# Performance work log

Measured on AMD Instinct MI355X. Metric: run time of the kernel, lower is better.

## Reference

```python
import jax, jax.numpy as jnp
import numpy as np

W = 5      # window size
H = 4      # num heads (num_channels)
EPS = 1e-6

def rmsnorm(x, w):
    return x * w * jax.lax.rsqrt(jnp.mean(x * x, axis=-1, keepdims=True) + EPS)

def dwconv3d(x, k):
    # x: [B,D0,D1,D2,C], k: [3,3,3,1,C] depthwise 3x3x3 conv, SAME padding
    return jax.lax.conv_general_dilated(
        x, k, (1, 1, 1), 'SAME',
        dimension_numbers=('NDHWC', 'DHWIO', 'NDHWC'),
        feature_group_count=x.shape[-1])

def _part(t):
    # [B,D0,D1,D2,C] -> [B*nw, W^3, C] non-overlapping 3D windows
    B, D0, D1, D2, C = t.shape
    t = t.reshape(B, D0 // W, W, D1 // W, W, D2 // W, W, C)
    t = t.transpose(0, 1, 3, 5, 2, 4, 6, 7)
    return t.reshape(-1, W ** 3, C)

def _unpart(t, B, D0, D1, D2):
    C = t.shape[-1]
    t = t.reshape(B, D0 // W, D1 // W, D2 // W, W, W, W, C)
    t = t.transpose(0, 1, 4, 2, 5, 3, 6, 7)
    return t.reshape(B, D0, D1, D2, C)

def _pool01(t):
    # mean-pool poolable_dims=(0,1) by factor W -> coarse grid
    B, D0, D1, D2, C = t.shape
    return t.reshape(B, D0 // W, W, D1 // W, W, D2, C).mean(axis=(2, 4))

def _mha(q, k, v):
    # q,k,v: [N, L, C] -> [N, L, C] multi-head attention
    N, L, C = q.shape
    dh = C // H
    q = q.reshape(N, L, H, dh)
    k = k.reshape(N, L, H, dh)
    v = v.reshape(N, L, H, dh)
    s = jnp.einsum('nqhd,nkhd->nhqk', q, k) * (1.0 / np.sqrt(dh))
    p = jax.nn.softmax(s, axis=-1)
    return jnp.einsum('nhqk,nkhd->nqhd', p, v).reshape(N, L, C)

def _hier_attn(x, qkv_w, qkv_b, proj_w, proj_b, dw_pre, dw_post, lr_down, lr_up):
    B, D0, D1, D2, C = x.shape
    # conv_position='both': pre depthwise-conv positional term
    xin = x + dwconv3d(x, dw_pre)
    qkv = xin @ qkv_w + qkv_b                     # [B,D0,D1,D2,3C]
    q, k, v = jnp.split(qkv, 3, axis=-1)
    # fine scale: windowed local attention in W^3 blocks
    fine = _unpart(_mha(_part(q), _part(k), _part(v)), B, D0, D1, D2)
    # coarse scale: pool dims (0,1) by W, global attention over coarse tokens
    qc, kc, vc = _pool01(q), _pool01(k), _pool01(v)
    Nc = qc.shape[1] * qc.shape[2] * qc.shape[3]
    oc = _mha(qc.reshape(B, Nc, C), kc.reshape(B, Nc, C), vc.reshape(B, Nc, C))
    oc = oc.reshape(B, D0 // W, D1 // W, D2, C)
    oc = jnp.repeat(jnp.repeat(oc, W, axis=1), W, axis=2)   # upsample to full grid
    # lowrank hierarchical merge of coarse branch into fine branch
    merged = fine + (oc @ lr_down) @ lr_up
    out = merged @ proj_w + proj_b
    out = out + xin                               # attn_residual
    out = out + dwconv3d(out, dw_post)            # post conv position
    return out

def setup_inputs() -> dict:
    key = jax.random.key(0)
    ks = jax.random.split(key, 8)
    B, D0, D1, D2, C = 4, 40, 40, 20, 256
    rank = C // 4
    s = 0.02
    return {
        'x': jax.random.normal(ks[0], (B, D0, D1, D2, C), jnp.float32),
        'norm1_w': jnp.ones((C,), jnp.float32),
        'attn_norm_w': jnp.ones((C,), jnp.float32),
        'qkv_w': jax.random.normal(ks[1], (C, 3 * C), jnp.float32) * s,
        'qkv_b': jnp.zeros((3 * C,), jnp.float32),
        'proj_w': jax.random.normal(ks[2], (C, C), jnp.float32) * s,
        'proj_b': jnp.zeros((C,), jnp.float32),
        'dw_pre': jax.random.normal(ks[3], (3, 3, 3, 1, C), jnp.float32) * s,
        'dw_post': jax.random.normal(ks[4], (3, 3, 3, 1, C), jnp.float32) * s,
        'lr_down': jax.random.normal(ks[5], (C, rank), jnp.float32) * s,
        'lr_up': jax.random.normal(ks[6], (rank, C), jnp.float32) * s,
    }

def reference(x, norm1_w, attn_norm_w, qkv_w, qkv_b, proj_w, proj_b,
              dw_pre, dw_post, lr_down, lr_up) -> jnp.ndarray:
    # x = x + attn_norm(hier_attn(norm1(x)))   (dropout inactive in eval)
    a = _hier_attn(rmsnorm(x, norm1_w), qkv_w, qkv_b, proj_w, proj_b,
                   dw_pre, dw_post, lr_down, lr_up)
    return x + rmsnorm(a, attn_norm_w)
```

## Files before the change

kernel.cpp:

```cpp
#include <hip/hip_runtime.h>

#define D0c 40
#define D1c 40
#define D2c 20
#define NVOX 128000

typedef __attribute__((ext_vector_type(4))) float f4;
typedef __attribute__((ext_vector_type(8))) __bf16 bf8;
typedef __attribute__((ext_vector_type(8))) unsigned short u8s;

static __device__ __forceinline__ unsigned short f2bf(float f) {
  union { float f; unsigned int u; } v; v.f = f;
  unsigned int r = v.u + 0x7fffu + ((v.u >> 16) & 1u);
  return (unsigned short)(r >> 16);
}
static __device__ __forceinline__ float bf2f(unsigned short h) {
  union { unsigned int u; float f; } v; v.u = ((unsigned int)h) << 16;
  return v.f;
}

#define MFMA16(a, b, c) __builtin_amdgcn_mfma_f32_16x16x32_bf16((a), (b), (c), 0, 0, 0)

static __device__ __forceinline__ void gload16(const void* g, void* l) {
  __builtin_amdgcn_global_load_lds((const __attribute__((address_space(1))) unsigned int*)g,
                                   (__attribute__((address_space(3))) unsigned int*)l, 16, 0, 0);
}

#define CONV_LOAD(NB, R)                                                      \
  do {                                                                        \
    _Pragma("unroll") for (int c = 0; c < 9; c++)                             \
        NB[c] = *(const ushort4*)(base[c] + (size_t)(R) * 256);               \
  } while (0)

#define CONV_CONSUME(NB)                                                      \
  do {                                                                        \
    f4 cf[9];                                                                 \
    _Pragma("unroll") for (int c = 0; c < 9; c++) {                           \
      cf[c].x = bf2f(NB[c].x); cf[c].y = bf2f(NB[c].y);                       \
      cf[c].z = bf2f(NB[c].z); cf[c].w = bf2f(NB[c].w);                       \
    }                                                                         \
    _Pragma("unroll") for (int c = 0; c < 9; c++) {                           \
      const f4 w0 = *(const f4*)&wl[(c * 3 + 0) * 256 + c0];                  \
      const f4 w1 = *(const f4*)&wl[(c * 3 + 1) * 256 + c0];                  \
      const f4 w2 = *(const f4*)&wl[(c * 3 + 2) * 256 + c0];                  \
      a0 += w2 * cf[c]; a1 += w1 * cf[c]; a2 += w0 * cf[c];                   \
    }                                                                         \
    a1 += cf[4];                                                              \
  } while (0)

#define CONV_SHIFT()                                                          \
  do { a0 = a1; a1 = a2; a2 = (f4){0.f, 0.f, 0.f, 0.f}; } while (0)

__global__ __launch_bounds__(256) void k_prepw(const float* __restrict__ qkv_w,
                                               const float* __restrict__ proj_w,
                                               unsigned short* __restrict__ wq,
                                               unsigned short* __restrict__ wp,
                                               unsigned short* __restrict__ zpad) {
  if (blockIdx.x == 1024) {
    u8s z = {0, 0, 0, 0, 0, 0, 0, 0};
    for (int i = threadIdx.x; i < 768; i += 256) *(u8s*)(zpad + i * 8) = z;
    return;
  }
  int id = blockIdx.x * 256 + threadIdx.x;
  if (id < 768 * 256) {
    int kk = id & 31, row = (id >> 5) & 127, kc = (id >> 12) & 7, nt = id >> 15;
    int s = kk >> 3, kj = kk & 7;
    int g = s ^ ((row >> 1) & 3);
    int k = kc * 32 + g * 8 + kj;
    int n = nt * 128 + row;
    wq[id] = f2bf(qkv_w[k * 768 + n]);
  } else {
    int j = id - 768 * 256;
    int kk = j & 31, row = (j >> 5) & 127, kc = (j >> 12) & 7, nt = j >> 15;
    int s = kk >> 3, kj = kk & 7;
    int g = s ^ ((row >> 1) & 3);
    int k = kc * 32 + g * 8 + kj;
    int n = nt * 128 + row;
    wp[j] = f2bf(proj_w[k * 256 + n]);
  }
}

__global__ __launch_bounds__(256) void k_rms1(const float* __restrict__ x,
                                              const float* __restrict__ w,
                                              unsigned short* __restrict__ xn) {
  int wv = threadIdx.x >> 6, ln = threadIdx.x & 63;
  int n = blockIdx.x * 4 + wv;
  f4 v = ((const f4*)(x + (size_t)n * 256))[ln];
  float ss = v.x * v.x + v.y * v.y + v.z * v.z + v.w * v.w;
#pragma unroll
  for (int m = 32; m >= 1; m >>= 1) ss += __shfl_xor(ss, m);
  float rs = rsqrtf(ss * (1.f / 256.f) + 1e-6f);
  f4 wv4 = ((const f4*)w)[ln];
  ushort4 o;
  o.x = f2bf(v.x * wv4.x * rs); o.y = f2bf(v.y * wv4.y * rs);
  o.z = f2bf(v.z * wv4.z * rs); o.w = f2bf(v.w * wv4.w * rs);
  ((ushort4*)(xn + (size_t)n * 256))[ln] = o;
}

__global__ __launch_bounds__(256) void k_convpre(const unsigned short* __restrict__ xn,
                                                 const float* __restrict__ dw,
                                                 const unsigned short* __restrict__ zpad,
                                                 unsigned short* __restrict__ xin) {
  __shared__ float wl[6912];
  for (int i = threadIdx.x; i < 6912; i += 256) wl[i] = dw[i];
  __syncthreads();
  int wv = threadIdx.x >> 6, ln = threadIdx.x & 63;
  int col = blockIdx.x * 4 + wv;
  int z1 = col % D1c; int t = col / D1c; int z0 = t % D0c; int b = t / D0c;
  int c0 = ln * 4;

  const unsigned short* base[9];
#pragma unroll
  for (int c = 0; c < 9; c++) {
    int dy = c / 3 - 1, dx = c % 3 - 1;
    int y0 = z0 + dy, y1 = z1 + dx;
    bool valid = ((unsigned)y0 < (unsigned)D0c) && ((unsigned)y1 < (unsigned)D1c);
    base[c] = valid ? (xn + ((size_t)((b * D0c + y0) * D1c + y1) * D2c) * 256 + c0)
                    : (zpad + c0);
  }
  f4 a0 = {0.f,0.f,0.f,0.f}, a1 = {0.f,0.f,0.f,0.f}, a2 = {0.f,0.f,0.f,0.f};
  ushort4 n0[9], n1[9];
  CONV_LOAD(n0, 0);
  CONV_LOAD(n1, 1);
  unsigned short* op = xin + ((size_t)col * D2c) * 256 + c0;

  CONV_CONSUME(n0);
  CONV_SHIFT();
  CONV_LOAD(n0, 2);
  CONV_CONSUME(n1);
  {
    ushort4 o;
    o.x = f2bf(a0.x); o.y = f2bf(a0.y); o.z = f2bf(a0.z); o.w = f2bf(a0.w);
    *(ushort4*)op = o; op += 256;
  }
  CONV_SHIFT();
  CONV_LOAD(n1, 3);

  for (int z = 2; z < 20; z += 2) {
    CONV_CONSUME(n0);
    {
      ushort4 o;
      o.x = f2bf(a0.x); o.y = f2bf(a0.y); o.z = f2bf(a0.z); o.w = f2bf(a0.w);
      *(ushort4*)op = o; op += 256;
    }
    CONV_SHIFT();
    int r2 = (z + 2 > 19) ? 19 : (z + 2);
    CONV_LOAD(n0, r2);

    CONV_CONSUME(n1);
    {
      ushort4 o;
      o.x = f2bf(a0.x); o.y = f2bf(a0.y); o.z = f2bf(a0.z); o.w = f2bf(a0.w);
      *(ushort4*)op = o; op += 256;
    }
    CONV_SHIFT();
    int r3 = (z + 3 > 19) ? 19 : (z + 3);
    CONV_LOAD(n1, r3);
  }
  {
    ushort4 o;
    o.x = f2bf(a0.x); o.y = f2bf(a0.y); o.z = f2bf(a0.z); o.w = f2bf(a0.w);
    *(ushort4*)op = o;
  }
}

__global__ __launch_bounds__(256) void k_gemm_qkv(const unsigned short* __restrict__ a_bf,
                                                  const unsigned short* __restrict__ wq2,
                                                  const float* __restrict__ bias,
                                                  unsigned short* __restrict__ out) {
  __shared__ unsigned short As[16384];
  __shared__ unsigned short Bs[8192];
  int m0 = blockIdx.x * 64;
  int tid = threadIdx.x;
  int w = tid >> 6, l = tid & 63;
  int wr = w >> 1, wc = w & 1;
  int lrow = l & 15, lg = l >> 4;

  {
    const char* Ab = (const char*)(a_bf + (size_t)m0 * 256);
    int row = tid >> 2, s = tid & 3;
    int g = s ^ ((row >> 1) & 3);
    const char* src0 = Ab + row * 512 + g * 16;
    char* dst0 = ((char*)As) + w * 1024 + l * 16;
#pragma unroll
    for (int kc = 0; kc < 8; kc++)
      gload16(src0 + kc * 64, dst0 + kc * 4096);
  }
  {
    const char* gB = (const char*)wq2;
    char* lB = (char*)Bs;
    gload16(gB + tid * 16, lB + w * 1024 + l * 16);
    gload16(gB + 4096 + tid * 16, lB + 4096 + w * 1024 + l * 16);
  }

  int buf = 0;
  f4 acc[2][4];
  for (int nt = 0; nt < 6; nt++) {
    float bvv[4];
#pragma unroll
    for (int j = 0; j < 4; j++) bvv[j] = bias[nt * 128 + wc * 64 + j * 16 + lrow];
#pragma unroll
    for (int i = 0; i < 2; i++)
#pragma unroll
      for (int j = 0; j < 4; j++) acc[i][j] = {0.f, 0.f, 0.f, 0.f};

    for (int kc = 0; kc < 8; kc++) {
      int t = nt * 8 + kc;
      if (t + 1 < 48) {
        const char* gB = (const char*)wq2 + (size_t)(t + 1) * 8192;
        char* lB = ((char*)Bs) + (buf ^ 1) * 8192;
        gload16(gB + tid * 16, lB + w * 1024 + l * 16);
        gload16(gB + 4096 + tid * 16, lB + 4096 + w * 1024 + l * 16);
        asm volatile("s_waitcnt vmcnt(2)\n\ts_barrier" ::: "memory");
      } else {
        asm volatile("s_waitcnt vmcnt(0)\n\ts_barrier" ::: "memory");
      }
      bf8 af[2], bf_[4];
#pragma unroll
      for (int i = 0; i < 2; i++) {
        int row = wr * 32 + i * 16 + lrow;
        af[i] = *(const bf8*)&As[kc * 2048 + row * 32 + ((lg ^ ((row >> 1) & 3)) * 8)];
      }
#pragma unroll
      for (int j = 0; j < 4; j++) {
        int rowb = wc * 64 + j * 16 + lrow;
        bf_[j] = *(const bf8*)&Bs[buf * 4096 + rowb * 32 + ((lg ^ ((rowb >> 1) & 3)) * 8)];
      }
#pragma unroll
      for (int i = 0; i < 2; i++)
#pragma unroll
        for (int j = 0; j < 4; j++) acc[i][j] = MFMA16(af[i], bf_[j], acc[i][j]);
      asm volatile("s_barrier" ::: "memory");
      buf ^= 1;
    }

    unsigned short* Cs = &Bs[(buf ^ 1) * 4096];
    int crow = tid >> 3, cseg = tid & 7;
#pragma unroll
    for (int h = 0; h < 2; h++) {
      if (wr == h) {
#pragma unroll
        for (int i = 0; i < 2; i++)
#pragma unroll
          for (int j = 0; j < 4; j++)
#pragma unroll
            for (int r = 0; r < 4; r++)
              Cs[(i * 16 + lg * 4 + r) * 128 + wc * 64 + j * 16 + lrow] =
                  f2bf(acc[i][j][r] + bvv[j]);
      }
      asm volatile("s_waitcnt lgkmcnt(0)\n\ts_barrier" ::: "memory");
      {
        u8s v0 = *(const u8s*)&Cs[crow * 128 + cseg * 16];
        u8s v1 = *(const u8s*)&Cs[crow * 128 + cseg * 16 + 8];
        unsigned short* orow = out + (size_t)(m0 + h * 32 + crow) * 768 + nt * 128 + cseg * 16;
        *(u8s*)orow = v0;
        *(u8s*)(orow + 8) = v1;
      }
      asm volatile("s_waitcnt lgkmcnt(0)\n\ts_barrier" ::: "memory");
    }
  }
}

__global__ __launch_bounds__(256) void k_fineattn(const unsigned short* __restrict__ qkv,
                                                  unsigned short* __restrict__ fine) {
  __shared__ unsigned short sm[27136];
  unsigned short* Qs = sm;
  unsigned short* Ks = sm + 9216;
  unsigned short* Vt = sm + 18432;
  unsigned short* Ps = sm;
  int h = blockIdx.x & 3, wid = blockIdx.x >> 2;
  int w2 = wid & 3, w1 = (wid >> 2) & 7, w0 = (wid >> 5) & 7, b = wid >> 8;
  int tid = threadIdx.x;
  int tok = tid >> 1, half = tid & 1;
  if (tok < 125) {
    int i0 = tok / 25, rr = tok % 25, i1 = rr / 5, i2 = rr % 5;
    int n = ((b * D0c + w0 * 5 + i0) * D1c + w1 * 5 + i1) * D2c + w2 * 5 + i2;
    const u8s* qp = (const u8s*)(qkv + (size_t)n * 768 + h * 64 + half * 32);
    const u8s* kp = (const u8s*)(qkv + (size_t)n * 768 + 256 + h * 64 + half * 32);
    const unsigned short* vp = qkv + (size_t)n * 768 + 512 + h * 64 + half * 32;
#pragma unroll
    for (int e = 0; e < 4; e++) {
      *(u8s*)&Qs[tok * 72 + half * 32 + e * 8] = qp[e];
      *(u8s*)&Ks[tok * 72 + half * 32 + e * 8] = kp[e];
    }
#pragma unroll
    for (int d = 0; d < 32; d++) Vt[(half * 32 + d) * 136 + tok] = vp[d];
  } else {
    u8s z = {0, 0, 0, 0, 0, 0, 0, 0};
#pragma unroll
    for (int e = 0; e < 4; e++) {
      *(u8s*)&Qs[tok * 72 + half * 32 + e * 8] = z;
      *(u8s*)&Ks[tok * 72 + half * 32 + e * 8] = z;
    }
#pragma unroll
    for (int d = 0; d < 32; d++) Vt[(half * 32 + d) * 136 + tok] = 0;
  }
  __syncthreads();
  int wv = tid >> 6, ln = tid & 63, lrow = ln & 15, lg = ln >> 4;
  f4 s[2][8];
#pragma unroll
  for (int mi = 0; mi < 2; mi++)
#pragma unroll
    for (int ni = 0; ni < 8; ni++) s[mi][ni] = {0.f, 0.f, 0.f, 0.f};
  bf8 aq[2][2];
#pragma unroll
  for (int ks = 0; ks < 2; ks++)
#pragma unroll
    for (int mi = 0; mi < 2; mi++)
      aq[mi][ks] = *(const bf8*)&Qs[(wv * 32 + mi * 16 + lrow) * 72 + ks * 32 + lg * 8];
#pragma unroll
  for (int ni = 0; ni < 8; ni++) {
#pragma unroll
    for (int ks = 0; ks < 2; ks++) {
      bf8 bk = *(const bf8*)&Ks[(ni * 16 + lrow) * 72 + ks * 32 + lg * 8];
      s[0][ni] = MFMA16(aq[0][ks], bk, s[0][ni]);
      s[1][ni] = MFMA16(aq[1][ks], bk, s[1][ni]);
    }
  }
#pragma unroll
  for (int mi = 0; mi < 2; mi++) {
#pragma unroll
    for (int j = 0; j < 4; j++) {
      float mx = -3e38f;
#pragma unroll
      for (int ni = 0; ni < 8; ni++) {
        int col = ni * 16 + lrow;
        float v = (col < 125) ? s[mi][ni][j] * 0.125f : -3e38f;
        s[mi][ni][j] = v;
        mx = fmaxf(mx, v);
      }
#pragma unroll
      for (int m = 8; m >= 1; m >>= 1) mx = fmaxf(mx, __shfl_xor(mx, m));
      float sum = 0.f;
#pragma unroll
      for (int ni = 0; ni < 8; ni++) {
        float p = __expf(s[mi][ni][j] - mx);
        s[mi][ni][j] = p;
        sum += p;
      }
#pragma unroll
      for (int m = 8; m >= 1; m >>= 1) sum += __shfl_xor(sum, m);
      float inv = 1.f / sum;
#pragma unroll
      for (int ni = 0; ni < 8; ni++) s[mi][ni][j] *= inv;
    }
  }
  __syncthreads();
#pragma unroll
  for (int mi = 0; mi < 2; mi++)
#pragma unroll
    for (int ni = 0; ni < 8; ni++)
#pragma unroll
      for (int j = 0; j < 4; j++)
        Ps[(wv * 32 + mi * 16 + lg * 4 + j) * 136 + ni * 16 + lrow] = f2bf(s[mi][ni][j]);
  __syncthreads();
  f4 o[2][4];
#pragma unroll
  for (int mi = 0; mi < 2; mi++)
#pragma unroll
    for (int ni = 0; ni < 4; ni++) o[mi][ni] = {0.f, 0.f, 0.f, 0.f};
#pragma unroll
  for (int ks = 0; ks < 4; ks++) {
    bf8 ap0 = *(const bf8*)&Ps[(wv * 32 + 0 + lrow) * 136 + ks * 32 + lg * 8];
    bf8 ap1 = *(const bf8*)&Ps[(wv * 32 + 16 + lrow) * 136 + ks * 32 + lg * 8];
#pragma unroll
    for (int ni = 0; ni < 4; ni++) {
      bf8 bv = *(const bf8*)&Vt[(ni * 16 + lrow) * 136 + ks * 32 + lg * 8];
      o[0][ni] = MFMA16(ap0, bv, o[0][ni]);
      o[1][ni] = MFMA16(ap1, bv, o[1][ni]);
    }
  }
#pragma unroll
  for (int mi = 0; mi < 2; mi++) {
    int rt0 = wv * 32 + mi * 16 + lg * 4;
#pragma unroll
    for (int r = 0; r < 4; r++) {
      int tk = rt0 + r;
      if (tk >= 125) continue;
      int i0 = tk / 25, rr = tk % 25, i1 = rr / 5, i2 = rr % 5;
      int n = ((b * D0c + w0 * 5 + i0) * D1c + w1 * 5 + i1) * D2c + w2 * 5 + i2;
#pragma unroll
      for (int ni = 0; ni < 4; ni++)
        fine[(size_t)n * 256 + h * 64 + ni * 16 + lrow] = f2bf(o[mi][ni][r]);
    }
  }
}

__global__ __launch_bounds__(128) void k_pool(const unsigned short* __restrict__ qkv,
                                              unsigned short* __restrict__ qc,
                                              unsigned short* __restrict__ kc,
                                              unsigned short* __restrict__ vct) {
  int ct = blockIdx.x;
  int tid = threadIdx.x;
  if (tid >= 96) return;
  int z2 = ct % 20; int t = ct / 20; int c1 = t & 7; int c0 = (t >> 3) & 7; int b = t >> 6;
  int off = tid * 8;
  f4 s0 = {0.f, 0.f, 0.f, 0.f}, s1 = {0.f, 0.f, 0.f, 0.f};
  for (int i0 = 0; i0 < 5; i0++)
    for (int i1 = 0; i1 < 5; i1++) {
      int n = ((b * D0c + c0 * 5 + i0) * D1c + c1 * 5 + i1) * D2c + z2;
      u8s v = *(const u8s*)(qkv + (size_t)n * 768 + off);
      s0.x += bf2f(v[0]); s0.y += bf2f(v[1]); s0.z += bf2f(v[2]); s0.w += bf2f(v[3]);
      s1.x += bf2f(v[4]); s1.y += bf2f(v[5]); s1.z += bf2f(v[6]); s1.w += bf2f(v[7]);
    }
  const float sc = 1.f / 25.f;
  s0.x *= sc; s0.y *= sc; s0.z *= sc; s0.w *= sc;
  s1.x *= sc; s1.y *= sc; s1.z *= sc; s1.w *= sc;
  if (off < 512) {
    unsigned short* dst = (off < 256) ? (qc + (size_t)ct * 256 + off)
                                      : (kc + (size_t)ct * 256 + (off - 256));
    u8s o;
    o[0] = f2bf(s0.x); o[1] = f2bf(s0.y); o[2] = f2bf(s0.z); o[3] = f2bf(s0.w);
    o[4] = f2bf(s1.x); o[5] = f2bf(s1.y); o[6] = f2bf(s1.z); o[7] = f2bf(s1.w);
    *(u8s*)dst = o;
  } else {
    int vch = off - 512;
    int h = vch >> 6, d0 = vch & 63;
    int tk = ct - b * 1280;
    unsigned short* vb = vct + (((size_t)b * 4 + h) * 64 + d0) * 1288 + tk;
    vb[0 * 1288] = f2bf(s0.x); vb[1 * 1288] = f2bf(s0.y);
    vb[2 * 1288] = f2bf(s0.z); vb[3 * 1288] = f2bf(s0.w);
    vb[4 * 1288] = f2bf(s1.x); vb[5 * 1288] = f2bf(s1.y);
    vb[6 * 1288] = f2bf(s1.z); vb[7 * 1288] = f2bf(s1.w);
  }
}

__global__ __launch_bounds__(256) void k_coarse(const unsigned short* __restrict__ qc,
                                                const unsigned short* __restrict__ kc,
                                                const unsigned short* __restrict__ vct,
                                                float* __restrict__ oc) {
  __shared__ unsigned short Qs[9216];
  __shared__ unsigned short KP[9216];
  __shared__ unsigned short Vts[4608];
  int qt = blockIdx.x;
  int b = blockIdx.y >> 2, h = blockIdx.y & 3;
  int tid = threadIdx.x, wv = tid >> 6, ln = tid & 63, lrow = ln & 15, lg = ln >> 4;
  {
    int tk = tid >> 1, half = tid & 1;
    const u8s* qp = (const u8s*)(qc + (size_t)(b * 1280 + qt * 128 + tk) * 256 + h * 64 + half * 32);
#pragma unroll
    for (int e = 0; e < 4; e++) *(u8s*)&Qs[tk * 72 + half * 32 + e * 8] = qp[e];
  }
  float mrun[2][4], srun[2][4];
  f4 o[2][4];
#pragma unroll
  for (int mi = 0; mi < 2; mi++)
#pragma unroll
    for (int j = 0; j < 4; j++) { mrun[mi][j] = -3e38f; srun[mi][j] = 0.f; }
#pragma unroll
  for (int mi = 0; mi < 2; mi++)
#pragma unroll
    for (int ni = 0; ni < 4; ni++) o[mi][ni] = {0.f, 0.f, 0.f, 0.f};

  int ktok = tid >> 2, kq = (tid & 3) * 16;
  int vd = tid >> 2, vtc = (tid & 3) * 16;

  for (int kt = 0; kt < 20; kt++) {
    {
      const u8s* kp = (const u8s*)(kc + (size_t)(b * 1280 + kt * 64 + ktok) * 256 + h * 64 + kq);
      *(u8s*)&KP[ktok * 72 + kq] = kp[0];
      *(u8s*)&KP[ktok * 72 + kq + 8] = kp[1];
      const u8s* vp = (const u8s*)(vct + (((size_t)b * 4 + h) * 64 + vd) * 1288 + kt * 64 + vtc);
      *(u8s*)&Vts[vd * 72 + vtc] = vp[0];
      *(u8s*)&Vts[vd * 72 + vtc + 8] = vp[1];
    }
    __syncthreads();
    f4 s[2][4];
#pragma unroll
    for (int mi = 0; mi < 2; mi++)
#pragma unroll
      for (int ni = 0; ni < 4; ni++) s[mi][ni] = {0.f, 0.f, 0.f, 0.f};
    bf8 aq[2][2];
#pragma unroll
    for (int ks = 0; ks < 2; ks++)
#pragma unroll
      for (int mi = 0; mi < 2; mi++)
        aq[mi][ks] = *(const bf8*)&Qs[(wv * 32 + mi * 16 + lrow) * 72 + ks * 32 + lg * 8];
#pragma unroll
    for (int ni = 0; ni < 4; ni++) {
#pragma unroll
      for (int ks = 0; ks < 2; ks++) {
        bf8 bk = *(const bf8*)&KP[(ni * 16 + lrow) * 72 + ks * 32 + lg * 8];
        s[0][ni] = MFMA16(aq[0][ks], bk, s[0][ni]);
        s[1][ni] = MFMA16(aq[1][ks], bk, s[1][ni]);
      }
    }
#pragma unroll
    for (int mi = 0; mi < 2; mi++) {
#pragma unroll
      for (int j = 0; j < 4; j++) {
        float mx = -3e38f;
#pragma unroll
        for (int ni = 0; ni < 4; ni++) {
          float v = s[mi][ni][j] * 0.125f;
          s[mi][ni][j] = v;
          mx = fmaxf(mx, v);
        }
#pragma unroll
        for (int m = 8; m >= 1; m >>= 1) mx = fmaxf(mx, __shfl_xor(mx, m));
        float nm = fmaxf(mrun[mi][j], mx);
        float alpha = __expf(mrun[mi][j] - nm);
        mrun[mi][j] = nm;
        float sum = 0.f;
#pragma unroll
        for (int ni = 0; ni < 4; ni++) {
          float p = __expf(s[mi][ni][j] - nm);
          s[mi][ni][j] = p;
          sum += p;
        }
#pragma unroll
        for (int m = 8; m >= 1; m >>= 1) sum += __shfl_xor(sum, m);
        srun[mi][j] = srun[mi][j] * alpha + sum;
#pragma unroll
        for (int ni = 0; ni < 4; ni++) o[mi][ni][j] *= alpha;
      }
    }
    __syncthreads();
#pragma unroll
    for (int mi = 0; mi < 2; mi++)
#pragma unroll
      for (int ni = 0; ni < 4; ni++)
#pragma unroll
        for (int j = 0; j < 4; j++)
          KP[(wv * 32 + mi * 16 + lg * 4 + j) * 72 + ni * 16 + lrow] = f2bf(s[mi][ni][j]);
    __syncthreads();
#pragma unroll
    for (int ks = 0; ks < 2; ks++) {
      bf8 ap0 = *(const bf8*)&KP[(wv * 32 + 0 + lrow) * 72 + ks * 32 + lg * 8];
      bf8 ap1 = *(const bf8*)&KP[(wv * 32 + 16 + lrow) * 72 + ks * 32 + lg * 8];
#pragma unroll
      for (int ni = 0; ni < 4; ni++) {
        bf8 bv = *(const bf8*)&Vts[(ni * 16 + lrow) * 72 + ks * 32 + lg * 8];
        o[0][ni] = MFMA16(ap0, bv, o[0][ni]);
        o[1][ni] = MFMA16(ap1, bv, o[1][ni]);
      }
    }
    __syncthreads();
  }
#pragma unroll
  for (int mi = 0; mi < 2; mi++)
#pragma unroll
    for (int j = 0; j < 4; j++) {
      float inv = 1.f / srun[mi][j];
      int row = qt * 128 + wv * 32 + mi * 16 + lg * 4 + j;
      float* orow = oc + ((size_t)(b * 1280 + row)) * 256 + h * 64;
#pragma unroll
      for (int ni = 0; ni < 4; ni++) orow[ni * 16 + lrow] = o[mi][ni][j] * inv;
    }
}

__global__ __launch_bounds__(256) void k_lowrank(const float* __restrict__ oc,
                                                 const float* __restrict__ lrd,
                                                 const float* __restrict__ lru,
                                                 float* __restrict__ oclr) {
  __shared__ float tmp[16 * 64];
  int t0 = blockIdx.x * 16;
  int tid = threadIdx.x;
  int i = tid >> 4, r4 = (tid & 15) * 4;
  f4 a = {0.f, 0.f, 0.f, 0.f};
  const float* orow = oc + (size_t)(t0 + i) * 256;
  for (int k = 0; k < 256; k++) {
    float ov = orow[k];
    const f4 w = *(const f4*)&lrd[k * 64 + r4];
    a.x += ov * w.x; a.y += ov * w.y; a.z += ov * w.z; a.w += ov * w.w;
  }
  *(f4*)&tmp[i * 64 + r4] = a;
  __syncthreads();
  int c16 = (tid & 15) * 16;
  f4 acc0 = {0.f,0.f,0.f,0.f}, acc1 = {0.f,0.f,0.f,0.f}, acc2 = {0.f,0.f,0.f,0.f}, acc3 = {0.f,0.f,0.f,0.f};
  for (int r = 0; r < 64; r++) {
    float tv = tmp[i * 64 + r];
    const f4* wr = (const f4*)&lru[r * 256 + c16];
    f4 w0 = wr[0], w1 = wr[1], w2 = wr[2], w3 = wr[3];
    acc0.x += tv * w0.x; acc0.y += tv * w0.y; acc0.z += tv * w0.z; acc0.w += tv * w0.w;
    acc1.x += tv * w1.x; acc1.y += tv * w1.y; acc1.z += tv * w1.z; acc1.w += tv * w1.w;
    acc2.x += tv * w2.x; acc2.y += tv * w2.y; acc2.z += tv * w2.z; acc2.w += tv * w2.w;
    acc3.x += tv * w3.x; acc3.y += tv * w3.y; acc3.z += tv * w3.z; acc3.w += tv * w3.w;
  }
  float* outr = oclr + (size_t)(t0 + i) * 256 + c16;
  *(f4*)&outr[0] = acc0; *(f4*)&outr[4] = acc1; *(f4*)&outr[8] = acc2; *(f4*)&outr[12] = acc3;
}

__global__ __launch_bounds__(256) void k_gemm_proj(const unsigned short* __restrict__ fine,
                                                   const float* __restrict__ oclr,
                                                   const unsigned short* __restrict__ wp2,
                                                   const float* __restrict__ bias,
                                                   const unsigned short* __restrict__ xin,
                                                   unsigned short* __restrict__ out1) {
  __shared__ unsigned short As[16384];
  __shared__ unsigned short Bs[8192];
  int m0 = blockIdx.x * 64;
  int tid = threadIdx.x;
  int w = tid >> 6, l = tid & 63;
  int wr = w >> 1, wc = w & 1;
  int lrow = l & 15, lg = l >> 4;

  {
    const char* gB = (const char*)wp2;
    char* lB = (char*)Bs;
    gload16(gB + tid * 16, lB + w * 1024 + l * 16);
    gload16(gB + 4096 + tid * 16, lB + 4096 + w * 1024 + l * 16);
  }
  {
    int row = tid >> 2, s = tid & 3;
    int g = s ^ ((row >> 1) & 3);
    int nrow = m0 + row;
    int z2 = nrow % D2c; int tt = nrow / D2c; int z1 = tt % D1c; tt /= D1c;
    int z0 = tt % D0c; int bb = tt / D0c;
    int ct = ((bb * 8 + z0 / 5) * 8 + z1 / 5) * 20 + z2;
    const unsigned short* fp = fine + (size_t)nrow * 256 + g * 8;
    const float* cp = oclr + (size_t)ct * 256 + g * 8;
#pragma unroll
    for (int kc = 0; kc < 8; kc++) {
      u8s fv = *(const u8s*)(fp + kc * 32);
      f4 cv0 = *(const f4*)(cp + kc * 32);
      f4 cv1 = *(const f4*)(cp + kc * 32 + 4);
      u8s t0;
      t0[0] = f2bf(bf2f(fv[0]) + cv0.x); t0[1] = f2bf(bf2f(fv[1]) + cv0.y);
      t0[2] = f2bf(bf2f(fv[2]) + cv0.z); t0[3] = f2bf(bf2f(fv[3]) + cv0.w);
      t0[4] = f2bf(bf2f(fv[4]) + cv1.x); t0[5] = f2bf(bf2f(fv[5]) + cv1.y);
      t0[6] = f2bf(bf2f(fv[6]) + cv1.z); t0[7] = f2bf(bf2f(fv[7]) + cv1.w);
      *(u8s*)&As[kc * 2048 + row * 32 + s * 8] = t0;
    }
  }
  asm volatile("s_waitcnt lgkmcnt(0)\n\ts_barrier" ::: "memory");

  int buf = 0;
  f4 acc[2][4];
  for (int nt = 0; nt < 2; nt++) {
    float bvv[4];
#pragma unroll
    for (int j = 0; j < 4; j++) bvv[j] = bias[nt * 128 + wc * 64 + j * 16 + lrow];
#pragma unroll
    for (int i = 0; i < 2; i++)
#pragma unroll
      for (int j = 0; j < 4; j++) acc[i][j] = {0.f, 0.f, 0.f, 0.f};

    for (int kc = 0; kc < 8; kc++) {
      int t = nt * 8 + kc;
      if (t + 1 < 16) {
        const char* gB = (const char*)wp2 + (size_t)(t + 1) * 8192;
        char* lB = ((char*)Bs) + (buf ^ 1) * 8192;
        gload16(gB + tid * 16, lB + w * 1024 + l * 16);
        gload16(gB + 4096 + tid * 16, lB + 4096 + w * 1024 + l * 16);
        asm volatile("s_waitcnt vmcnt(2)\n\ts_barrier" ::: "memory");
      } else {
        asm volatile("s_waitcnt vmcnt(0)\n\ts_barrier" ::: "memory");
      }
      bf8 af[2], bf_[4];
#pragma unroll
      for (int i = 0; i < 2; i++) {
        int row = wr * 32 + i * 16 + lrow;
        af[i] = *(const bf8*)&As[kc * 2048 + row * 32 + ((lg ^ ((row >> 1) & 3)) * 8)];
      }
#pragma unroll
      for (int j = 0; j < 4; j++) {
        int rowb = wc * 64 + j * 16 + lrow;
        bf_[j] = *(const bf8*)&Bs[buf * 4096 + rowb * 32 + ((lg ^ ((rowb >> 1) & 3)) * 8)];
      }
#pragma unroll
      for (int i = 0; i < 2; i++)
#pragma unroll
        for (int j = 0; j < 4; j++) acc[i][j] = MFMA16(af[i], bf_[j], acc[i][j]);
      asm volatile("s_barrier" ::: "memory");
      buf ^= 1;
    }

    unsigned short* Cs = &Bs[(buf ^ 1) * 4096];
    int crow = tid >> 3, cseg = tid & 7;
#pragma unroll
    for (int h = 0; h < 2; h++) {
      if (wr == h) {
#pragma unroll
        for (int i = 0; i < 2; i++)
#pragma unroll
          for (int j = 0; j < 4; j++)
#pragma unroll
            for (int r = 0; r < 4; r++)
              Cs[(i * 16 + lg * 4 + r) * 128 + wc * 64 + j * 16 + lrow] =
                  f2bf(acc[i][j][r] + bvv[j]);
      }
      asm volatile("s_waitcnt lgkmcnt(0)\n\ts_barrier" ::: "memory");
      {
        u8s v0 = *(const u8s*)&Cs[crow * 128 + cseg * 16];
        u8s v1 = *(const u8s*)&Cs[crow * 128 + cseg * 16 + 8];
        const unsigned short* xrow = xin + (size_t)(m0 + h * 32 + crow) * 256 + nt * 128 + cseg * 16;
        u8s x0 = *(const u8s*)xrow;
        u8s x1 = *(const u8s*)(xrow + 8);
        u8s o0, o1;
#pragma unroll
        for (int e = 0; e < 8; e++) {
          o0[e] = f2bf(bf2f(v0[e]) + bf2f(x0[e]));
          o1[e] = f2bf(bf2f(v1[e]) + bf2f(x1[e]));
        }
        unsigned short* orow = out1 + (size_t)(m0 + h * 32 + crow) * 256 + nt * 128 + cseg * 16;
        *(u8s*)orow = o0;
        *(u8s*)(orow + 8) = o1;
      }
      asm volatile("s_waitcnt lgkmcnt(0)\n\ts_barrier" ::: "memory");
    }
  }
}

__global__ __launch_bounds__(256) void k_convpost(const unsigned short* __restrict__ o1,
                                                  const float* __restrict__ dw,
                                                  const unsigned short* __restrict__ zpad,
                                                  const float* __restrict__ x,
                                                  const float* __restrict__ anw,
                                                  float* __restrict__ outp) {
  __shared__ float wl[6912];
  for (int i = threadIdx.x; i < 6912; i += 256) wl[i] = dw[i];
  __syncthreads();
  int wv = threadIdx.x >> 6, ln = threadIdx.x & 63;
  int col = blockIdx.x * 4 + wv;
  int z1 = col % D1c; int t = col / D1c; int z0 = t % D0c; int b = t / D0c;
  int c0 = ln * 4;

  const unsigned short* base[9];
#pragma unroll
  for (int c = 0; c < 9; c++) {
    int dy = c / 3 - 1, dx = c % 3 - 1;
    int y0 = z0 + dy, y1 = z1 + dx;
    bool valid = ((unsigned)y0 < (unsigned)D0c) && ((unsigned)y1 < (unsigned)D1c);
    base[c] = valid ? (o1 + ((size_t)((b * D0c + y0) * D1c + y1) * D2c) * 256 + c0)
                    : (zpad + c0);
  }
  f4 a0 = {0.f,0.f,0.f,0.f}, a1 = {0.f,0.f,0.f,0.f}, a2 = {0.f,0.f,0.f,0.f};
  ushort4 n0[9], n1[9];
  CONV_LOAD(n0, 0);
  CONV_LOAD(n1, 1);
  const f4 wv4 = *(const f4*)(anw + c0);
  const float* xp = x + ((size_t)col * D2c) * 256 + c0;
  float* op = outp + ((size_t)col * D2c) * 256 + c0;

#define POST_STORE()                                                          \
  do {                                                                        \
    float ss = a0.x * a0.x + a0.y * a0.y + a0.z * a0.z + a0.w * a0.w;         \
    _Pragma("unroll") for (int m = 32; m >= 1; m >>= 1)                       \
        ss += __shfl_xor(ss, m);                                              \
    float rs = rsqrtf(ss * (1.f / 256.f) + 1e-6f);                            \
    f4 xv = *(const f4*)xp;                                                   \
    f4 res;                                                                   \
    res.x = xv.x + a0.x * wv4.x * rs;                                         \
    res.y = xv.y + a0.y * wv4.y * rs;                                         \
    res.z = xv.z + a0.z * wv4.z * rs;                                         \
    res.w = xv.w + a0.w * wv4.w * rs;                                         \
    *(f4*)op = res;                                                           \
    xp += 256; op += 256;                                                     \
  } while (0)

  CONV_CONSUME(n0);
  CONV_SHIFT();
  CONV_LOAD(n0, 2);
  CONV_CONSUME(n1);
  POST_STORE();
  CONV_SHIFT();
  CONV_LOAD(n1, 3);

  for (int z = 2; z < 20; z += 2) {
    CONV_CONSUME(n0);
    POST_STORE();
    CONV_SHIFT();
    int r2 = (z + 2 > 19) ? 19 : (z + 2);
    CONV_LOAD(n0, r2);

    CONV_CONSUME(n1);
    POST_STORE();
    CONV_SHIFT();
    int r3 = (z + 3 > 19) ? 19 : (z + 3);
    CONV_LOAD(n1, r3);
  }
  POST_STORE();
#undef POST_STORE
}

extern "C" void kernel_launch(void* const* d_in, const int* in_sizes, int n_in,
                              void* d_out, int out_size, void* d_ws, size_t ws_size,
                              hipStream_t stream) {
  const float* x          = (const float*)d_in[0];
  const float* norm1_w    = (const float*)d_in[1];
  const float* attn_norm_w= (const float*)d_in[2];
  const float* qkv_w      = (const float*)d_in[3];
  const float* qkv_b      = (const float*)d_in[4];
  const float* proj_w     = (const float*)d_in[5];
  const float* proj_b     = (const float*)d_in[6];
  const float* dw_pre     = (const float*)d_in[7];
  const float* dw_post    = (const float*)d_in[8];
  const float* lr_down    = (const float*)d_in[9];
  const float* lr_up      = (const float*)d_in[10];
  float* outp = (float*)d_out;

  unsigned char* w = (unsigned char*)d_ws;
  size_t off = 0;
  unsigned short* xn   = (unsigned short*)(w + off); off += 65536000ULL;
  unsigned short* xin  = (unsigned short*)(w + off); off += 65536000ULL;
  unsigned short* qkv  = (unsigned short*)(w + off); off += 196608000ULL;
  unsigned short* out1 = (unsigned short*)(w + off); off += 65536000ULL;
  unsigned short* qc   = (unsigned short*)(w + off); off += 2621440ULL;
  unsigned short* kc   = (unsigned short*)(w + off); off += 2621440ULL;
  unsigned short* vct  = (unsigned short*)(w + off); off += 2637824ULL;
  float* oc            = (float*)(w + off);          off += 5242880ULL;
  float* oclr          = (float*)(w + off);          off += 5242880ULL;
  unsigned short* wq   = (unsigned short*)(w + off); off += 393216ULL;
  unsigned short* wp   = (unsigned short*)(w + off); off += 131072ULL;
  unsigned short* zpad = (unsigned short*)(w + off); off += 12288ULL;
  unsigned short* fine = xn;

  k_prepw<<<1025, 256, 0, stream>>>(qkv_w, proj_w, wq, wp, zpad);
  k_rms1<<<32000, 256, 0, stream>>>(x, norm1_w, xn);
  k_convpre<<<1600, 256, 0, stream>>>(xn, dw_pre, zpad, xin);
  k_gemm_qkv<<<2000, 256, 0, stream>>>(xin, wq, qkv_b, qkv);
  k_fineattn<<<4096, 256, 0, stream>>>(qkv, fine);
  k_pool<<<5120, 128, 0, stream>>>(qkv, qc, kc, vct);
  k_coarse<<<dim3(10, 16), 256, 0, stream>>>(qc, kc, vct, oc);
  k_lowrank<<<320, 256, 0, stream>>>(oc, lr_down, lr_up, oclr);
  k_gemm_proj<<<2000, 256, 0, stream>>>(fine, oclr, wp, proj_b, xin, out1);
  k_convpost<<<1600, 256, 0, stream>>>(out1, dw_post, zpad, x, attn_norm_w, outp);
}
```

Before: 617.3 us.

## Load QKV GEMM operands directly from global into registers, dropping LDS staging

The QKV projection GEMM no longer stages A and B tiles through shared memory with async global-to-LDS loads and double buffering. Each wave now keeps its A fragments in registers for the whole kernel and reads B fragments straight from global memory, so the weight prep no longer applies the LDS bank-swizzle. This removes the per-k-step barriers and LDS traffic, but relies on L1/L2 caching of the weight tensor and raises register pressure. Global loads are exposed to latency without explicit prefetch.

```diff
diff --git a/kernel.cpp b/kernel.cpp
--- a/kernel.cpp
+++ b/kernel.cpp
@@ -64,9 +64,7 @@
   int id = blockIdx.x * 256 + threadIdx.x;
   if (id < 768 * 256) {
     int kk = id & 31, row = (id >> 5) & 127, kc = (id >> 12) & 7, nt = id >> 15;
-    int s = kk >> 3, kj = kk & 7;
-    int g = s ^ ((row >> 1) & 3);
-    int k = kc * 32 + g * 8 + kj;
+    int k = kc * 32 + kk;
     int n = nt * 128 + row;
     wq[id] = f2bf(qkv_w[k * 768 + n]);
   } else {
@@ -168,74 +166,45 @@
                                                   const unsigned short* __restrict__ wq2,
                                                   const float* __restrict__ bias,
                                                   unsigned short* __restrict__ out) {
-  __shared__ unsigned short As[16384];
-  __shared__ unsigned short Bs[8192];
+  __shared__ unsigned short Cs[4096];
   int m0 = blockIdx.x * 64;
   int tid = threadIdx.x;
   int w = tid >> 6, l = tid & 63;
   int wr = w >> 1, wc = w & 1;
   int lrow = l & 15, lg = l >> 4;
 
-  {
-    const char* Ab = (const char*)(a_bf + (size_t)m0 * 256);
-    int row = tid >> 2, s = tid & 3;
-    int g = s ^ ((row >> 1) & 3);
-    const char* src0 = Ab + row * 512 + g * 16;
-    char* dst0 = ((char*)As) + w * 1024 + l * 16;
+  bf8 afr[16];
+#pragma unroll
+  for (int i = 0; i < 2; i++)
 #pragma unroll
     for (int kc = 0; kc < 8; kc++)
-      gload16(src0 + kc * 64, dst0 + kc * 4096);
-  }
-  {
-    const char* gB = (const char*)wq2;
-    char* lB = (char*)Bs;
-    gload16(gB + tid * 16, lB + w * 1024 + l * 16);
-    gload16(gB + 4096 + tid * 16, lB + 4096 + w * 1024 + l * 16);
-  }
-
-  int buf = 0;
-  f4 acc[2][4];
+      afr[i * 8 + kc] = *(const bf8*)(a_bf +
+          (size_t)(m0 + wr * 32 + i * 16 + lrow) * 256 + kc * 32 + lg * 8);
+
+  int crow = tid >> 3, cseg = tid & 7;
   for (int nt = 0; nt < 6; nt++) {
     float bvv[4];
 #pragma unroll
     for (int j = 0; j < 4; j++) bvv[j] = bias[nt * 128 + wc * 64 + j * 16 + lrow];
+    f4 acc[2][4];
 #pragma unroll
     for (int i = 0; i < 2; i++)
 #pragma unroll
       for (int j = 0; j < 4; j++) acc[i][j] = {0.f, 0.f, 0.f, 0.f};
 
+    const unsigned short* Bnt = wq2 + (size_t)nt * 32768;
+#pragma unroll
     for (int kc = 0; kc < 8; kc++) {
-      int t = nt * 8 + kc;
-      if (t + 1 < 48) {
-        const char* gB = (const char*)wq2 + (size_t)(t + 1) * 8192;
-        char* lB = ((char*)Bs) + (buf ^ 1) * 8192;
-        gload16(gB + tid * 16, lB + w * 1024 + l * 16);
-        gload16(gB + 4096 + tid * 16, lB + 4096 + w * 1024 + l * 16);
-        asm volatile("s_waitcnt vmcnt(2)\n\ts_barrier" ::: "memory");
-      } else {
-        asm volatile("s_waitcnt vmcnt(0)\n\ts_barrier" ::: "memory");
-      }
-      bf8 af[2], bf_[4];
-#pragma unroll
-      for (int i = 0; i < 2; i++) {
-        int row = wr * 32 + i * 16 + lrow;
-        af[i] = *(const bf8*)&As[kc * 2048 + row * 32 + ((lg ^ ((row >> 1) & 3)) * 8)];
-      }
-#pragma unroll
-      for (int j = 0; j < 4; j++) {
-        int rowb = wc * 64 + j * 16 + lrow;
-        bf_[j] = *(const bf8*)&Bs[buf * 4096 + rowb * 32 + ((lg ^ ((rowb >> 1) & 3)) * 8)];
-      }
+      bf8 bfj[4];
+#pragma unroll
+      for (int j = 0; j < 4; j++)
+        bfj[j] = *(const bf8*)(Bnt + kc * 4096 + (wc * 64 + j * 16 + lrow) * 32 + lg * 8);
 #pragma unroll
       for (int i = 0; i < 2; i++)
 #pragma unroll
-        for (int j = 0; j < 4; j++) acc[i][j] = MFMA16(af[i], bf_[j], acc[i][j]);
-      asm volatile("s_barrier" ::: "memory");
-      buf ^= 1;
-    }
-
-    unsigned short* Cs = &Bs[(buf ^ 1) * 4096];
-    int crow = tid >> 3, cseg = tid & 7;
+        for (int j = 0; j < 4; j++) acc[i][j] = MFMA16(afr[i * 8 + kc], bfj[j], acc[i][j]);
+    }
+
 #pragma unroll
     for (int h = 0; h < 2; h++) {
       if (wr == h) {
@@ -248,7 +217,7 @@
               Cs[(i * 16 + lg * 4 + r) * 128 + wc * 64 + j * 16 + lrow] =
                   f2bf(acc[i][j][r] + bvv[j]);
       }
-      asm volatile("s_waitcnt lgkmcnt(0)\n\ts_barrier" ::: "memory");
+      __syncthreads();
       {
         u8s v0 = *(const u8s*)&Cs[crow * 128 + cseg * 16];
         u8s v1 = *(const u8s*)&Cs[crow * 128 + cseg * 16 + 8];
@@ -256,7 +225,7 @@
         *(u8s*)orow = v0;
         *(u8s*)(orow + 8) = v1;
       }
-      asm volatile("s_waitcnt lgkmcnt(0)\n\ts_barrier" ::: "memory");
+      __syncthreads();
     }
   }
 }
```

Measured after the change: 636.0 us. +3.0%, slower.
